# Kernel optimization log

Measured on AMD Instinct MI355X. Metric: run time of the kernel, lower is better.

Reference implementation:

```python
import jax, jax.numpy as jnp
import numpy as np

B, S, D, H, DFF, NL, VOCAB, SRC = 16, 128, 768, 12, 3072, 6, 32000, 256


def _pe_table():
    pos = np.arange(S)[:, None].astype(np.float32)
    div = np.exp(np.arange(0, D, 2).astype(np.float32) * (-np.log(10000.0) / D))
    pe = np.zeros((S, D), np.float32)
    pe[:, 0::2] = np.sin(pos * div)
    pe[:, 1::2] = np.cos(pos * div)
    return jnp.asarray(pe)


def _ln(x, a, b, eps=1e-6):
    m = jnp.mean(x, axis=-1, keepdims=True)
    v = jnp.mean((x - m) ** 2, axis=-1, keepdims=True)
    return a * (x - m) / jnp.sqrt(v + eps) + b


def _mha(q_in, k_in, v_in, mask, Wq, bq, Wk, bk, Wv, bv, Wo, bo):
    Bq, Sq, Dm = q_in.shape
    Sk = k_in.shape[1]
    dk = Dm // H
    q = (q_in @ Wq + bq).reshape(Bq, Sq, H, dk).transpose(0, 2, 1, 3)
    k = (k_in @ Wk + bk).reshape(Bq, Sk, H, dk).transpose(0, 2, 1, 3)
    v = (v_in @ Wv + bv).reshape(Bq, Sk, H, dk).transpose(0, 2, 1, 3)
    s = jnp.einsum('bhqd,bhkd->bhqk', q, k) / jnp.sqrt(jnp.float32(dk))
    if mask is not None:
        s = jnp.where(mask == 0, jnp.float32(-1e9), s)
    a = jax.nn.softmax(s, axis=-1)
    o = jnp.einsum('bhqk,bhkd->bhqd', a, v).transpose(0, 2, 1, 3).reshape(Bq, Sq, Dm)
    return o @ Wo + bo


def _combined_mask(trg):
    # Vectorized, faithful replica of create_combined_mask (incl. its cumulative
    # cross-batch zeroing: for j in 0..B-2, if padding_start[j]!=0 zero rows
    # >= padding_start[j] of ALL batches b >= j).
    b, s = trg.shape
    is_pad = (trg == 0)
    haspad = jnp.any(is_pad, axis=1)
    start = jnp.where(haspad, jnp.argmax(is_pad, axis=1), 0)  # first pad idx, 0 if none
    c = jnp.where(start == 0, s + 1, start)                   # sentinel = never cut
    cmin = jax.lax.cummin(c)
    r = cmin[jnp.minimum(jnp.arange(b), b - 2)]               # effective cutoff per batch
    look = jnp.tril(jnp.ones((s, s), jnp.float32))
    keep = (jnp.arange(s)[None, :] < r[:, None]).astype(jnp.float32)  # (B,S) rows kept
    return (look[None] * keep[:, :, None])[:, None]           # (B,1,S,S)


def setup_inputs():
    key = jax.random.key(0)
    ks = jax.random.split(key, 16)
    tok = jax.random.randint(ks[0], (B, S), 1, VOCAB)
    lens = jax.random.randint(ks[1], (B,), S // 2, S + 1)
    trg = jnp.where(jnp.arange(S)[None, :] < lens[:, None], tok, 0).astype(jnp.int32)
    e_outputs = jax.random.normal(ks[2], (B, SRC, D), dtype=jnp.float32)
    src_mask = jax.random.randint(ks[3], (B, 1, 1, SRC), 0, 2).at[..., 0].set(1).astype(jnp.int32)
    w = lambda k, shape: (jax.random.normal(k, shape) * 0.02).astype(jnp.float32)
    emb = (jax.random.normal(ks[4], (VOCAB, D)) * 0.1).astype(jnp.float32).at[0].set(0.0)
    return {
        'trg': trg, 'e_outputs': e_outputs, 'src_mask': src_mask,
        'emb': emb,
        'y_param': jax.random.normal(ks[5], (S, D), dtype=jnp.float32),
        'pe_alpha': jnp.float32(1.0),
        'Wq': w(ks[6], (NL, 3, D, D)), 'Wk': w(ks[7], (NL, 3, D, D)),
        'Wv': w(ks[8], (NL, 3, D, D)), 'Wo': w(ks[9], (NL, 3, D, D)),
        'bq': jnp.zeros((NL, 3, D)), 'bk': jnp.zeros((NL, 3, D)),
        'bv': jnp.zeros((NL, 3, D)), 'bo': jnp.zeros((NL, 3, D)),
        'W1': w(ks[10], (NL, D, DFF)), 'b1': jnp.zeros((NL, DFF)),
        'W2': w(ks[11], (NL, DFF, D)), 'b2': jnp.zeros((NL, D)),
        'ln_a': jnp.ones((NL, 5, D)), 'ln_b': jnp.zeros((NL, 5, D)),
        'final_a': jnp.ones((D,)), 'final_b': jnp.zeros((D,)),
    }


def reference(trg, e_outputs, src_mask, emb, y_param, pe_alpha, Wq, Wk, Wv, Wo,
              bq, bk, bv, bo, W1, b1, W2, b2, ln_a, ln_b, final_a, final_b):
    x = emb[trg] + pe_alpha * _pe_table()            # embedding + scaled PE
    y = jnp.broadcast_to(y_param, (trg.shape[0],) + y_param.shape)
    trg_mask = _combined_mask(trg)
    for i in range(Wq.shape[0]):
        x2 = _ln(x, ln_a[i, 0], ln_b[i, 0])
        x = x + _mha(x2, x2, x2, trg_mask, Wq[i, 0], bq[i, 0], Wk[i, 0], bk[i, 0], Wv[i, 0], bv[i, 0], Wo[i, 0], bo[i, 0])
        y2 = _ln(y, ln_a[i, 1], ln_b[i, 1])
        y = y + _mha(y2, e_outputs, e_outputs, src_mask, Wq[i, 1], bq[i, 1], Wk[i, 1], bk[i, 1], Wv[i, 1], bv[i, 1], Wo[i, 1], bo[i, 1])
        x2 = _ln(x, ln_a[i, 2], ln_b[i, 2])
        y3 = _ln(y, ln_a[i, 3], ln_b[i, 3])
        x = x + _mha(x2, y3, y3, None, Wq[i, 2], bq[i, 2], Wk[i, 2], bk[i, 2], Wv[i, 2], bv[i, 2], Wo[i, 2], bo[i, 2])
        x2 = _ln(x, ln_a[i, 4], ln_b[i, 4])
        x = x + jnp.maximum(x2 @ W1[i] + b1[i], 0.0) @ W2[i] + b2[i]
    return _ln(x, final_a, final_b)
```

## Files before the change

### kernel.cpp

```cpp
#include <hip/hip_runtime.h>

#define BB 16
#define SS 128
#define DD 768
#define HH 12
#define DKK 64
#define DFFF 3072
#define NLL 6
#define SRCC 256

typedef short bf16x8 __attribute__((ext_vector_type(8)));
typedef float f32x4 __attribute__((ext_vector_type(4)));
typedef unsigned short us8 __attribute__((ext_vector_type(8)));
typedef unsigned short us4 __attribute__((ext_vector_type(4)));

__device__ __forceinline__ unsigned short f2bf(float f) {
  unsigned int u = __builtin_bit_cast(unsigned int, f);
  u = (u + 0x7fff + ((u >> 16) & 1)) >> 16;
  return (unsigned short)u;
}

#define GLOADLDS16(gp, lp)                                              \
  __builtin_amdgcn_global_load_lds(                                     \
      (const __attribute__((address_space(1))) void*)(gp),              \
      (__attribute__((address_space(3))) void*)(lp), 16, 0, 0)

__global__ void pe_build_k(float* __restrict__ pe) {
  int idx = blockIdx.x * blockDim.x + threadIdx.x;
  if (idx >= SS * (DD / 2)) return;
  int s = idx / (DD / 2);
  int i = idx - s * (DD / 2);
  float div = expf((float)(2 * i) * (-logf(10000.0f) / (float)DD));
  float ang = (float)s * div;
  pe[s * DD + 2 * i]     = sinf(ang);
  pe[s * DD + 2 * i + 1] = cosf(ang);
}

__global__ void embjoint_k(const int* __restrict__ trg, const float* __restrict__ emb,
                           const float* __restrict__ pe, const float* __restrict__ alpha,
                           const float* __restrict__ yp,
                           float* __restrict__ x, float* __restrict__ y) {
  int idx = blockIdx.x * blockDim.x + threadIdx.x;
  int c = idx % (DD / 4);
  int r = idx / (DD / 4);
  if (r >= BB * SS) return;
  int s = r % SS;
  if (blockIdx.y == 0) {
    float al = alpha[0];
    float4 e = *(const float4*)(emb + (size_t)trg[r] * DD + c * 4);
    float4 p = *(const float4*)(pe + (size_t)s * DD + c * 4);
    float4 o;
    o.x = e.x + al * p.x; o.y = e.y + al * p.y;
    o.z = e.z + al * p.z; o.w = e.w + al * p.w;
    *(float4*)(x + (size_t)r * DD + c * 4) = o;
  } else {
    *(float4*)(y + (size_t)r * DD + c * 4) = *(const float4*)(yp + (size_t)s * DD + c * 4);
  }
}

__global__ void mb_k(const int* __restrict__ trg, int* __restrict__ rbuf,
                     const float* __restrict__ bq, const float* __restrict__ bk,
                     const float* __restrict__ bv, float* __restrict__ bqkv1,
                     float* __restrict__ bkv2, float* __restrict__ bqkv3) {
  int t = threadIdx.x;
  if (blockIdx.x == 0) {
    __shared__ int first[BB];
    if (t < BB) first[t] = 0x7fffffff;
    __syncthreads();
    int b = t >> 4, p0 = (t & 15) * 8;
    int loc = 0x7fffffff;
#pragma unroll
    for (int i = 0; i < 8; i++) {
      if (trg[b * SS + p0 + i] == 0) { loc = p0 + i; break; }
    }
    atomicMin(&first[b], loc);
    __syncthreads();
    if (t == 0) {
      int cmin = 0x7fffffff;
      int cm[BB];
      for (int bb = 0; bb < BB; bb++) {
        int start = (first[bb] == 0x7fffffff) ? 0 : first[bb];
        int c = (start == 0) ? (SS + 1) : start;
        cmin = min(cmin, c);
        cm[bb] = cmin;
      }
      for (int bb = 0; bb < BB; bb++) rbuf[bb] = cm[min(bb, BB - 2)];
    }
    return;
  }
  int i = (blockIdx.x - 1) * 256 + t;
  if (i >= NLL * 6144) return;
  int l = i / 6144, j = i - l * 6144;
  if (j < 2304) {
    int s = j / 768, c = j - s * 768;
    const float* src = (s == 0) ? bq : (s == 1 ? bk : bv);
    bqkv1[l * 2304 + j] = src[(l * 3 + 0) * 768 + c];
  } else if (j < 3840) {
    int jj = j - 2304;
    int s = jj / 768, c = jj - s * 768;
    bkv2[l * 1536 + jj] = ((s == 0) ? bk : bv)[(l * 3 + 1) * 768 + c];
  } else {
    int jj = j - 3840;
    int s = jj / 768, c = jj - s * 768;
    const float* src = (s == 0) ? bq : (s == 1 ? bk : bv);
    bqkv3[l * 2304 + jj] = src[(l * 3 + 2) * 768 + c];
  }
}

__global__ __launch_bounds__(256) void ln_k(const float* __restrict__ x,
                                            const float* __restrict__ ga,
                                            const float* __restrict__ gb,
                                            float* __restrict__ out) {
  __shared__ float sm[8];
  int row = blockIdx.x;
  int t = threadIdx.x;
  const float* xr = x + (size_t)row * DD;
  float v0 = xr[t], v1 = xr[t + 256], v2 = xr[t + 512];
  float s = v0 + v1 + v2;
#pragma unroll
  for (int o = 32; o > 0; o >>= 1) s += __shfl_down(s, o);
  if ((t & 63) == 0) sm[t >> 6] = s;
  __syncthreads();
  float mean = (sm[0] + sm[1] + sm[2] + sm[3]) * (1.0f / (float)DD);
  float d0 = v0 - mean, d1 = v1 - mean, d2 = v2 - mean;
  float q = d0 * d0 + d1 * d1 + d2 * d2;
#pragma unroll
  for (int o = 32; o > 0; o >>= 1) q += __shfl_down(q, o);
  if ((t & 63) == 0) sm[4 + (t >> 6)] = q;
  __syncthreads();
  float var = (sm[4] + sm[5] + sm[6] + sm[7]) * (1.0f / (float)DD);
  float inv = 1.0f / sqrtf(var + 1e-6f);
  float* orow = out + (size_t)row * DD;
  orow[t]       = ga[t] * d0 * inv + gb[t];
  orow[t + 256] = ga[t + 256] * d1 * inv + gb[t + 256];
  orow[t + 512] = ga[t + 512] * d2 * inv + gb[t + 512];
}

__device__ __forceinline__ void lnb_body(const float* __restrict__ xr,
                                         const float* __restrict__ ga,
                                         const float* __restrict__ gb,
                                         unsigned short* __restrict__ orow,
                                         float* sm, int t) {
  float v0 = xr[t], v1 = xr[t + 256], v2 = xr[t + 512];
  float s = v0 + v1 + v2;
#pragma unroll
  for (int o = 32; o > 0; o >>= 1) s += __shfl_down(s, o);
  if ((t & 63) == 0) sm[t >> 6] = s;
  __syncthreads();
  float mean = (sm[0] + sm[1] + sm[2] + sm[3]) * (1.0f / (float)DD);
  float d0 = v0 - mean, d1 = v1 - mean, d2 = v2 - mean;
  float q = d0 * d0 + d1 * d1 + d2 * d2;
#pragma unroll
  for (int o = 32; o > 0; o >>= 1) q += __shfl_down(q, o);
  if ((t & 63) == 0) sm[4 + (t >> 6)] = q;
  __syncthreads();
  float var = (sm[4] + sm[5] + sm[6] + sm[7]) * (1.0f / (float)DD);
  float inv = 1.0f / sqrtf(var + 1e-6f);
  orow[t]       = f2bf(ga[t] * d0 * inv + gb[t]);
  orow[t + 256] = f2bf(ga[t + 256] * d1 * inv + gb[t + 256]);
  orow[t + 512] = f2bf(ga[t + 512] * d2 * inv + gb[t + 512]);
}

__global__ __launch_bounds__(256) void lnb_k(const float* __restrict__ x,
                                             const float* __restrict__ ga,
                                             const float* __restrict__ gb,
                                             unsigned short* __restrict__ out) {
  __shared__ float sm[8];
  int row = blockIdx.x;
  lnb_body(x + (size_t)row * DD, ga, gb, out + (size_t)row * DD, sm, threadIdx.x);
}

__global__ __launch_bounds__(256) void lnb2_k(const float* __restrict__ x,
                                              const float* __restrict__ y,
                                              const float* __restrict__ ga2,
                                              const float* __restrict__ gb2,
                                              const float* __restrict__ ga3,
                                              const float* __restrict__ gb3,
                                              unsigned short* __restrict__ ox,
                                              unsigned short* __restrict__ oy) {
  __shared__ float sm[8];
  int row = blockIdx.x;
  if (row < BB * SS)
    lnb_body(x + (size_t)row * DD, ga2, gb2, ox + (size_t)row * DD, sm, threadIdx.x);
  else {
    row -= BB * SS;
    lnb_body(y + (size_t)row * DD, ga3, gb3, oy + (size_t)row * DD, sm, threadIdx.x);
  }
}

__device__ __forceinline__ void wt_tile(const float* __restrict__ s,
                                        unsigned short* __restrict__ d,
                                        int K, int N, int k0, int n0,
                                        float (*tl)[65], int t) {
  int rr = t >> 4, cc = (t & 15) * 4;
#pragma unroll
  for (int i = 0; i < 4; i++) {
    int row = rr + i * 16;
    float4 v = *(const float4*)(s + (size_t)(k0 + row) * N + n0 + cc);
    tl[row][cc + 0] = v.x; tl[row][cc + 1] = v.y;
    tl[row][cc + 2] = v.z; tl[row][cc + 3] = v.w;
  }
  __syncthreads();
  int kchunk = t & 7, nrow = t >> 3;
#pragma unroll
  for (int p = 0; p < 2; p++) {
    int n = p * 32 + nrow;
    us8 o;
#pragma unroll
    for (int j = 0; j < 8; j++) o[j] = f2bf(tl[kchunk * 8 + j][n]);
    *(us8*)(d + (size_t)(n0 + n) * K + k0 + kchunk * 8) = o;
  }
}

__global__ __launch_bounds__(256) void wt_k(const float* __restrict__ src,
                                            unsigned short* __restrict__ dst,
                                            int K, int N) {
  __shared__ float tl[64][65];
  wt_tile(src + (size_t)blockIdx.z * K * N, dst + (size_t)blockIdx.z * K * N,
          K, N, blockIdx.y * 64, blockIdx.x * 64, tl, threadIdx.x);
}

__global__ __launch_bounds__(256) void wtall_k(
    const float* __restrict__ Wq, const float* __restrict__ Wk,
    const float* __restrict__ Wv, const float* __restrict__ Wo,
    unsigned short* __restrict__ wqkv1A, unsigned short* __restrict__ wq2A,
    unsigned short* __restrict__ wkv2A, unsigned short* __restrict__ wqkv3A,
    unsigned short* __restrict__ wotA) {
  __shared__ float tl[64][65];
  const size_t M1 = (size_t)DD * DD;
  int z = blockIdx.z;
  int l = z / 12, m = z - l * 12;
  size_t s3 = (size_t)l * 3 * M1;
  const float* s;
  unsigned short* d;
  switch (m) {
    case 0:  s = Wq + s3;          d = wqkv1A + l * 3 * M1;          break;
    case 1:  s = Wk + s3;          d = wqkv1A + l * 3 * M1 + M1;     break;
    case 2:  s = Wv + s3;          d = wqkv1A + l * 3 * M1 + 2 * M1; break;
    case 3:  s = Wq + s3 + M1;     d = wq2A + l * M1;                break;
    case 4:  s = Wk + s3 + M1;     d = wkv2A + l * 2 * M1;           break;
    case 5:  s = Wv + s3 + M1;     d = wkv2A + l * 2 * M1 + M1;      break;
    case 6:  s = Wq + s3 + 2 * M1; d = wqkv3A + l * 3 * M1;          break;
    case 7:  s = Wk + s3 + 2 * M1; d = wqkv3A + l * 3 * M1 + M1;     break;
    case 8:  s = Wv + s3 + 2 * M1; d = wqkv3A + l * 3 * M1 + 2 * M1; break;
    case 9:  s = Wo + s3;          d = wotA + l * 3 * M1;            break;
    case 10: s = Wo + s3 + M1;     d = wotA + l * 3 * M1 + M1;       break;
    default: s = Wo + s3 + 2 * M1; d = wotA + l * 3 * M1 + 2 * M1;   break;
  }
  wt_tile(s, d, DD, DD, blockIdx.y * 64, blockIdx.x * 64, tl, threadIdx.x);
}

__global__ void cvt_k(const float* __restrict__ s, unsigned short* __restrict__ d, int n8) {
  int i = blockIdx.x * blockDim.x + threadIdx.x;
  if (i >= n8) return;
  float4 a = *(const float4*)(s + (size_t)i * 8);
  float4 b = *(const float4*)(s + (size_t)i * 8 + 4);
  us8 o;
  o[0] = f2bf(a.x); o[1] = f2bf(a.y); o[2] = f2bf(a.z); o[3] = f2bf(a.w);
  o[4] = f2bf(b.x); o[5] = f2bf(b.y); o[6] = f2bf(b.z); o[7] = f2bf(b.w);
  *(us8*)(d + (size_t)i * 8) = o;
}

template <int BM>
__global__ __launch_bounds__(256) void mgemm_k(
    const unsigned short* __restrict__ A0, const unsigned short* __restrict__ A1,
    const unsigned short* __restrict__ Bt, const float* __restrict__ bias,
    const float* __restrict__ res, void* __restrict__ C,
    unsigned short* __restrict__ hd0, unsigned short* __restrict__ hd1,
    unsigned short* __restrict__ hd2,
    int sh0, int sh1, int sh2, int M, int N, int K, int flags, int vtbits) {
  constexpr int FM = BM / 32;
  constexpr int HB = BM / 2;
  __shared__ unsigned short As[BM * 32];
  __shared__ unsigned short Bs[64 * 32];
  int t = threadIdx.x;
  int wave = t >> 6, lane = t & 63;
  int m0 = blockIdx.y * BM, n0 = blockIdx.x * 64;
  int seg = n0 / 768;
  const unsigned short* A = (seg == 0) ? A0 : A1;
  int wm = wave >> 1, wn = wave & 1;
  f32x4 acc[FM][2] = {};
  int aRow = t >> 2, aC8 = (t & 3) * 8;
  const unsigned short* Ab = A + (size_t)m0 * K + aC8;
  const unsigned short* Bb = Bt + (size_t)n0 * K + aC8;
  int aOff0 = (wm * HB + (lane & 15)) * 32 + (lane >> 4) * 8;
  int bOff0 = (wn * 32 + (lane & 15)) * 32 + (lane >> 4) * 8;
  for (int k0 = 0; k0 < K; k0 += 32) {
#pragma unroll
    for (int h = 0; h < BM / 64; h++)
      GLOADLDS16(Ab + (size_t)(h * 64 + aRow) * K + k0, As + h * 2048 + wave * 512);
    GLOADLDS16(Bb + (size_t)aRow * K + k0, Bs + wave * 512);
    __syncthreads();
    bf16x8 aF[FM], bF[2];
#pragma unroll
    for (int fm = 0; fm < FM; fm++)
      aF[fm] = *(const bf16x8*)(As + aOff0 + fm * 16 * 32);
#pragma unroll
    for (int fn = 0; fn < 2; fn++)
      bF[fn] = *(const bf16x8*)(Bs + bOff0 + fn * 16 * 32);
#pragma unroll
    for (int fm = 0; fm < FM; fm++)
#pragma unroll
      for (int fn = 0; fn < 2; fn++)
        acc[fm][fn] = __builtin_amdgcn_mfma_f32_16x16x32_bf16(aF[fm], bF[fn], acc[fm][fn], 0, 0, 0);
    __syncthreads();
  }
  int lcol = lane & 15, lrow4 = (lane >> 4) * 4;
  bool hm = (flags & 4) != 0;
  unsigned short* hd = nullptr;
  int sh = 0, segBase = seg * 768, vtseg = 0;
  if (hm) {
    hd = (seg == 0) ? hd0 : (seg == 1 ? hd1 : hd2);
    sh = (seg == 0) ? sh0 : (seg == 1 ? sh1 : sh2);
    vtseg = (vtbits >> seg) & 1;
  }
#pragma unroll
  for (int fm = 0; fm < FM; fm++) {
#pragma unroll
    for (int fn = 0; fn < 2; fn++) {
      int col = n0 + wn * 32 + fn * 16 + lcol;
      float bv = bias[col];
      int rowb = m0 + wm * HB + fm * 16 + lrow4;
      if (hm) {
        int colr = col - segBase;
        int hh = colr >> 6, dd = colr & 63;
        int bb = rowb >> sh, ssb = rowb & ((1 << sh) - 1);
        if (vtseg) {
          size_t idx = (((size_t)bb * HH + hh) * 64 + dd) * (size_t)(1 << sh) + ssb;
          us4 pk;
#pragma unroll
          for (int r = 0; r < 4; r++) pk[r] = f2bf(acc[fm][fn][r] + bv);
          *(us4*)(hd + idx) = pk;
        } else {
          size_t base = ((((size_t)bb * HH + hh) << sh) + ssb) * 64 + dd;
#pragma unroll
          for (int r = 0; r < 4; r++) hd[base + (size_t)r * 64] = f2bf(acc[fm][fn][r] + bv);
        }
      } else {
#pragma unroll
        for (int r = 0; r < 4; r++) {
          int row = rowb + r;
          float v = acc[fm][fn][r] + bv;
          size_t idx = (size_t)row * N + col;
          if (res) v += res[idx];
          if (flags & 1) v = fmaxf(v, 0.f);
          if (flags & 2) ((unsigned short*)C)[idx] = f2bf(v);
          else ((float*)C)[idx] = v;
        }
      }
    }
  }
}

template <int SK>
__global__ __launch_bounds__(256) void attn3_k(const unsigned short* __restrict__ qh,
                                               const unsigned short* __restrict__ kh,
                                               const unsigned short* __restrict__ vth,
                                               unsigned short* __restrict__ ctxb, int mode,
                                               const int* __restrict__ rbuf,
                                               const int* __restrict__ smask) {
  constexpr int NPH = SK / 128;
  constexpr int NF = SK / 16;
  __shared__ unsigned short kvb[128 * 72];
  __shared__ unsigned short pbuf[64 * (SK + 8)];
  int qhalf = blockIdx.x, h = blockIdx.y, b = blockIdx.z;
  int t = threadIdx.x;
  int wave = t >> 6, lane = t & 63;
  int l15 = lane & 15, lhi = lane >> 4;
  int qrow0 = qhalf * 64 + wave * 16;
  size_t bh = (size_t)b * HH + h;
  bf16x8 aQ[2];
#pragma unroll
  for (int ks = 0; ks < 2; ks++)
    aQ[ks] = *(const bf16x8*)(qh + (bh * SS + qrow0 + l15) * 64 + ks * 32 + lhi * 8);
  f32x4 accS[NF] = {};
  const unsigned short* kbase = kh + bh * SK * 64;
  for (int ph = 0; ph < NPH; ph++) {
    if (ph) __syncthreads();
    {
      int c0 = t * 4;
#pragma unroll
      for (int i = 0; i < 4; i++) {
        int c = c0 + i, row = c >> 3, co = (c & 7) * 8;
        *(us8*)&kvb[row * 72 + co] = *(const us8*)(kbase + (size_t)(ph * 128 + row) * 64 + co);
      }
    }
    __syncthreads();
#pragma unroll
    for (int kf = 0; kf < 8; kf++) {
      int gf = ph * 8 + kf;
#pragma unroll
      for (int ks = 0; ks < 2; ks++) {
        bf16x8 bK = *(const bf16x8*)(&kvb[(kf * 16 + l15) * 72 + ks * 32 + lhi * 8]);
        accS[gf] = __builtin_amdgcn_mfma_f32_16x16x32_bf16(aQ[ks], bK, accS[gf], 0, 0, 0);
      }
    }
  }
  int rcut = (mode == 0) ? rbuf[b] : 0;
#pragma unroll
  for (int r = 0; r < 4; r++) {
    int qg = qrow0 + lhi * 4 + r;
    float mx = -3.4e38f;
#pragma unroll
    for (int gf = 0; gf < NF; gf++) {
      int k = gf * 16 + l15;
      float s = accS[gf][r] * 0.125f;
      bool keep = true;
      if (mode == 0) keep = (k <= qg) && (qg < rcut);
      else if (mode == 1) keep = (smask[b * SRCC + k] != 0);
      s = keep ? s : -1e9f;
      accS[gf][r] = s;
      mx = fmaxf(mx, s);
    }
#pragma unroll
    for (int o = 1; o < 16; o <<= 1) mx = fmaxf(mx, __shfl_xor(mx, o));
    float sum = 0.f;
#pragma unroll
    for (int gf = 0; gf < NF; gf++) {
      float e = expf(accS[gf][r] - mx);
      accS[gf][r] = e;
      sum += e;
    }
#pragma unroll
    for (int o = 1; o < 16; o <<= 1) sum += __shfl_xor(sum, o);
    float rinv = 1.0f / sum;
#pragma unroll
    for (int gf = 0; gf < NF; gf++) accS[gf][r] *= rinv;
  }
#pragma unroll
  for (int gf = 0; gf < NF; gf++) {
#pragma unroll
    for (int r = 0; r < 4; r++) {
      int ql = wave * 16 + lhi * 4 + r;
      pbuf[ql * (SK + 8) + gf * 16 + l15] = f2bf(accS[gf][r]);
    }
  }
  __syncthreads();
  f32x4 accO[4] = {};
  const unsigned short* vbase = vth + bh * 64 * SK;
  for (int ph = 0; ph < NPH; ph++) {
    if (ph) __syncthreads();
    {
      int c0 = t * 4;
#pragma unroll
      for (int i = 0; i < 4; i++) {
        int c = c0 + i, row = c >> 4, co = (c & 15) * 8;
        *(us8*)&kvb[row * 136 + co] = *(const us8*)(vbase + (size_t)row * SK + ph * 128 + co);
      }
    }
    __syncthreads();
#pragma unroll
    for (int ks = 0; ks < 4; ks++) {
      bf16x8 aP = *(const bf16x8*)(&pbuf[(wave * 16 + l15) * (SK + 8) + ph * 128 + ks * 32 + lhi * 8]);
#pragma unroll
      for (int nf = 0; nf < 4; nf++) {
        bf16x8 bV = *(const bf16x8*)(&kvb[(nf * 16 + l15) * 136 + ks * 32 + lhi * 8]);
        accO[nf] = __builtin_amdgcn_mfma_f32_16x16x32_bf16(aP, bV, accO[nf], 0, 0, 0);
      }
    }
  }
#pragma unroll
  for (int nf = 0; nf < 4; nf++) {
#pragma unroll
    for (int r = 0; r < 4; r++) {
      int qg = qrow0 + lhi * 4 + r;
      ctxb[((size_t)b * SS + qg) * DD + h * 64 + nf * 16 + l15] = f2bf(accO[nf][r]);
    }
  }
}

extern "C" void kernel_launch(void* const* d_in, const int* in_sizes, int n_in,
                              void* d_out, int out_size, void* d_ws, size_t ws_size,
                              hipStream_t stream) {
  const int*   trg   = (const int*)d_in[0];
  const float* e_out = (const float*)d_in[1];
  const int*   smask = (const int*)d_in[2];
  const float* emb   = (const float*)d_in[3];
  const float* ypar  = (const float*)d_in[4];
  const float* alpha = (const float*)d_in[5];
  const float* Wq = (const float*)d_in[6];
  const float* Wk = (const float*)d_in[7];
  const float* Wv = (const float*)d_in[8];
  const float* Wo = (const float*)d_in[9];
  const float* bq = (const float*)d_in[10];
  const float* bk = (const float*)d_in[11];
  const float* bv = (const float*)d_in[12];
  const float* bo = (const float*)d_in[13];
  const float* W1 = (const float*)d_in[14];
  const float* b1 = (const float*)d_in[15];
  const float* W2 = (const float*)d_in[16];
  const float* b2 = (const float*)d_in[17];
  const float* lna = (const float*)d_in[18];
  const float* lnbp = (const float*)d_in[19];
  const float* fa = (const float*)d_in[20];
  const float* fb = (const float*)d_in[21];
  float* out = (float*)d_out;

  float* ws = (float*)d_ws;
  size_t off = 0;
  auto alloc = [&](size_t n) { float* p = ws + off; off += n; return p; };
  const size_t M1 = (size_t)DD * DD;
  float* pe  = alloc((size_t)SS * DD);
  int* rbuf  = (int*)alloc(64);
  float* x   = alloc((size_t)BB * SS * DD);
  float* y   = alloc((size_t)BB * SS * DD);
  float* bqkv1 = alloc((size_t)NLL * 2304);
  float* bkv2  = alloc((size_t)NLL * 1536);
  float* bqkv3 = alloc((size_t)NLL * 2304);
  unsigned short* qhb  = (unsigned short*)alloc((size_t)BB * HH * SS * DKK / 2);
  unsigned short* khb  = (unsigned short*)alloc((size_t)BB * HH * SRCC * DKK / 2);
  unsigned short* vthb = (unsigned short*)alloc((size_t)BB * HH * SRCC * DKK / 2);
  unsigned short* x2b   = (unsigned short*)alloc((size_t)BB * SS * DD / 2);
  unsigned short* y3b   = (unsigned short*)alloc((size_t)BB * SS * DD / 2);
  unsigned short* ctxb  = (unsigned short*)alloc((size_t)BB * SS * DD / 2);
  unsigned short* midb  = (unsigned short*)alloc((size_t)BB * SS * DFFF / 2);
  unsigned short* eob   = (unsigned short*)alloc((size_t)BB * SRCC * DD / 2);
  unsigned short* wqkv1A = (unsigned short*)alloc((size_t)NLL * 3 * M1 / 2);
  unsigned short* wq2A   = (unsigned short*)alloc((size_t)NLL * M1 / 2);
  unsigned short* wkv2A  = (unsigned short*)alloc((size_t)NLL * 2 * M1 / 2);
  unsigned short* wqkv3A = (unsigned short*)alloc((size_t)NLL * 3 * M1 / 2);
  unsigned short* wotA   = (unsigned short*)alloc((size_t)NLL * 3 * M1 / 2);
  unsigned short* w1tA   = (unsigned short*)alloc((size_t)NLL * DD * DFFF / 2);
  unsigned short* w2tA   = (unsigned short*)alloc((size_t)NLL * DFFF * DD / 2);
  if (ws_size < off * sizeof(float)) return;

  pe_build_k<<<(SS * (DD / 2) + 255) / 256, 256, 0, stream>>>(pe);
  embjoint_k<<<dim3((BB * SS * (DD / 4) + 255) / 256, 2), 256, 0, stream>>>(
      trg, emb, pe, alpha, ypar, x, y);
  mb_k<<<1 + (NLL * 6144 + 255) / 256, 256, 0, stream>>>(trg, rbuf, bq, bk, bv,
                                                         bqkv1, bkv2, bqkv3);
  cvt_k<<<(BB * SRCC * DD / 8 + 255) / 256, 256, 0, stream>>>(e_out, eob, BB * SRCC * DD / 8);
  wtall_k<<<dim3(12, 12, NLL * 12), 256, 0, stream>>>(Wq, Wk, Wv, Wo,
                                                      wqkv1A, wq2A, wkv2A, wqkv3A, wotA);
  wt_k<<<dim3(48, 12, NLL), 256, 0, stream>>>(W1, w1tA, DD, DFFF);
  wt_k<<<dim3(12, 48, NLL), 256, 0, stream>>>(W2, w2tA, DFFF, DD);

  auto MG128 = [&](const unsigned short* A0, const unsigned short* A1, int M, int K,
                   const unsigned short* Bt, int N, const float* bias, const float* res,
                   void* C, unsigned short* h0, unsigned short* h1, unsigned short* h2,
                   int s0, int s1, int s2, int flags, int vtb) {
    mgemm_k<128><<<dim3(N / 64, M / 128), 256, 0, stream>>>(A0, A1, Bt, bias, res, C,
                                                            h0, h1, h2, s0, s1, s2, M, N, K, flags, vtb);
  };
  auto MG64 = [&](const unsigned short* A0, int M, int K,
                  const unsigned short* Bt, int N, const float* bias, const float* res,
                  void* C, unsigned short* h0, int s0, int flags, int vtb) {
    mgemm_k<64><<<dim3(N / 64, M / 64), 256, 0, stream>>>(A0, A0, Bt, bias, res, C,
                                                          h0, nullptr, nullptr, s0, 0, 0, M, N, K, flags, vtb);
  };
  const dim3 agrid(SS / 64, HH, BB);

  for (int l = 0; l < NLL; l++) {
    auto LNB = [&](const float* in, int slot, unsigned short* o) {
      lnb_k<<<BB * SS, 256, 0, stream>>>(in, lna + ((size_t)l * 5 + slot) * DD,
                                         lnbp + ((size_t)l * 5 + slot) * DD, o);
    };
    LNB(x, 0, x2b);
    MG128(x2b, x2b, BB * SS, DD, wqkv1A + l * 3 * M1, 2304, bqkv1 + l * 2304, nullptr,
          nullptr, qhb, khb, vthb, 7, 7, 7, 4, 0b100);
    attn3_k<SS><<<agrid, 256, 0, stream>>>(qhb, khb, vthb, ctxb, 0, rbuf, nullptr);
    MG64(ctxb, BB * SS, DD, wotA + l * 3 * M1, DD, bo + ((size_t)l * 3 + 0) * DD, x, x,
         nullptr, 0, 0, 0);
    LNB(y, 1, x2b);
    MG64(x2b, BB * SS, DD, wq2A + l * M1, DD, bq + ((size_t)l * 3 + 1) * DD, nullptr,
         nullptr, qhb, 7, 4, 1 * 0);
    MG128(eob, eob, BB * SRCC, DD, wkv2A + l * 2 * M1, 1536, bkv2 + l * 1536, nullptr,
          nullptr, khb, vthb, nullptr, 8, 8, 0, 4, 0b10);
    attn3_k<SRCC><<<agrid, 256, 0, stream>>>(qhb, khb, vthb, ctxb, 1, nullptr, smask);
    MG64(ctxb, BB * SS, DD, wotA + l * 3 * M1 + M1, DD, bo + ((size_t)l * 3 + 1) * DD, y, y,
         nullptr, 0, 0, 0);
    lnb2_k<<<2 * BB * SS, 256, 0, stream>>>(x, y,
        lna + ((size_t)l * 5 + 2) * DD, lnbp + ((size_t)l * 5 + 2) * DD,
        lna + ((size_t)l * 5 + 3) * DD, lnbp + ((size_t)l * 5 + 3) * DD, x2b, y3b);
    MG128(x2b, y3b, BB * SS, DD, wqkv3A + l * 3 * M1, 2304, bqkv3 + l * 2304, nullptr,
          nullptr, qhb, khb, vthb, 7, 7, 7, 4, 0b100);
    attn3_k<SS><<<agrid, 256, 0, stream>>>(qhb, khb, vthb, ctxb, 2, nullptr, nullptr);
    MG64(ctxb, BB * SS, DD, wotA + l * 3 * M1 + 2 * M1, DD, bo + ((size_t)l * 3 + 2) * DD, x, x,
         nullptr, 0, 0, 0);
    LNB(x, 4, x2b);
    MG128(x2b, x2b, BB * SS, DD, w1tA + (size_t)l * DD * DFFF, DFFF, b1 + (size_t)l * DFFF,
          nullptr, midb, nullptr, nullptr, nullptr, 0, 0, 0, 3, 0);
    MG64(midb, BB * SS, DFFF, w2tA + (size_t)l * DFFF * DD, DD, b2 + (size_t)l * DD, x, x,
         nullptr, 0, 0, 0);
  }
  ln_k<<<BB * SS, 256, 0, stream>>>(x, fa, fb, out);
}
```

Measured before the change: 1.653 ms.

## Batch independent self/cross attention branches and precompute cross-attention K/V for all layers

The self-attention and cross-attention branches in each layer are independent, so their LayerNorms, Q/QKV projections and output projections are now fused into shared launches (lnb2_k, qkvq_k, wob_k). The encoder K/V projections for all six layers are computed up front in one large GEMM launch instead of once per layer. All weight transposes and the e_out conversion are merged into a single kernel with larger tiles, and the PE table is computed inline during embedding. This cuts launch count and gives small GEMMs more blocks for occupancy, at the cost of extra workspace for per-layer K/V buffers.

```diff
diff --git a/kernel.cpp b/kernel.cpp
--- a/kernel.cpp
+++ b/kernel.cpp
@@ -1,4 +1,5 @@
 #include <hip/hip_runtime.h>
+#include <math.h>
 
 #define BB 16
 #define SS 128
@@ -25,19 +26,8 @@
       (const __attribute__((address_space(1))) void*)(gp),              \
       (__attribute__((address_space(3))) void*)(lp), 16, 0, 0)
 
-__global__ void pe_build_k(float* __restrict__ pe) {
-  int idx = blockIdx.x * blockDim.x + threadIdx.x;
-  if (idx >= SS * (DD / 2)) return;
-  int s = idx / (DD / 2);
-  int i = idx - s * (DD / 2);
-  float div = expf((float)(2 * i) * (-logf(10000.0f) / (float)DD));
-  float ang = (float)s * div;
-  pe[s * DD + 2 * i]     = sinf(ang);
-  pe[s * DD + 2 * i + 1] = cosf(ang);
-}
-
 __global__ void embjoint_k(const int* __restrict__ trg, const float* __restrict__ emb,
-                           const float* __restrict__ pe, const float* __restrict__ alpha,
+                           const float* __restrict__ alpha,
                            const float* __restrict__ yp,
                            float* __restrict__ x, float* __restrict__ y) {
   int idx = blockIdx.x * blockDim.x + threadIdx.x;
@@ -48,10 +38,15 @@
   if (blockIdx.y == 0) {
     float al = alpha[0];
     float4 e = *(const float4*)(emb + (size_t)trg[r] * DD + c * 4);
-    float4 p = *(const float4*)(pe + (size_t)s * DD + c * 4);
+    float coef = -logf(10000.0f) / (float)DD;
+    float div0 = expf((float)(4 * c) * coef);
+    float div1 = expf((float)(4 * c + 2) * coef);
+    float s0, c0, s1, c1;
+    sincosf((float)s * div0, &s0, &c0);
+    sincosf((float)s * div1, &s1, &c1);
     float4 o;
-    o.x = e.x + al * p.x; o.y = e.y + al * p.y;
-    o.z = e.z + al * p.z; o.w = e.w + al * p.w;
+    o.x = e.x + al * s0; o.y = e.y + al * c0;
+    o.z = e.z + al * s1; o.w = e.w + al * c1;
     *(float4*)(x + (size_t)r * DD + c * 4) = o;
   } else {
     *(float4*)(y + (size_t)r * DD + c * 4) = *(const float4*)(yp + (size_t)s * DD + c * 4);
@@ -172,93 +167,156 @@
 
 __global__ __launch_bounds__(256) void lnb2_k(const float* __restrict__ x,
                                               const float* __restrict__ y,
-                                              const float* __restrict__ ga2,
-                                              const float* __restrict__ gb2,
-                                              const float* __restrict__ ga3,
-                                              const float* __restrict__ gb3,
+                                              const float* __restrict__ gax,
+                                              const float* __restrict__ gbx,
+                                              const float* __restrict__ gay,
+                                              const float* __restrict__ gby,
                                               unsigned short* __restrict__ ox,
                                               unsigned short* __restrict__ oy) {
   __shared__ float sm[8];
   int row = blockIdx.x;
   if (row < BB * SS)
-    lnb_body(x + (size_t)row * DD, ga2, gb2, ox + (size_t)row * DD, sm, threadIdx.x);
+    lnb_body(x + (size_t)row * DD, gax, gbx, ox + (size_t)row * DD, sm, threadIdx.x);
   else {
     row -= BB * SS;
-    lnb_body(y + (size_t)row * DD, ga3, gb3, oy + (size_t)row * DD, sm, threadIdx.x);
-  }
-}
-
-__device__ __forceinline__ void wt_tile(const float* __restrict__ s,
+    lnb_body(y + (size_t)row * DD, gay, gby, oy + (size_t)row * DD, sm, threadIdx.x);
+  }
+}
+
+__device__ __forceinline__ void tr_tile(const float* __restrict__ s,
                                         unsigned short* __restrict__ d,
                                         int K, int N, int k0, int n0,
-                                        float (*tl)[65], int t) {
-  int rr = t >> 4, cc = (t & 15) * 4;
+                                        float (*tl)[69], int t) {
+#pragma unroll
+  for (int i = 0; i < 8; i++) {
+    int c = t + i * 256;
+    int row = c >> 4, c4 = (c & 15) * 4;
+    float4 v = *(const float4*)(s + (size_t)(k0 + row) * N + n0 + c4);
+    tl[row][c4 + 0] = v.x; tl[row][c4 + 1] = v.y;
+    tl[row][c4 + 2] = v.z; tl[row][c4 + 3] = v.w;
+  }
+  __syncthreads();
 #pragma unroll
   for (int i = 0; i < 4; i++) {
-    int row = rr + i * 16;
-    float4 v = *(const float4*)(s + (size_t)(k0 + row) * N + n0 + cc);
-    tl[row][cc + 0] = v.x; tl[row][cc + 1] = v.y;
-    tl[row][cc + 2] = v.z; tl[row][cc + 3] = v.w;
-  }
-  __syncthreads();
-  int kchunk = t & 7, nrow = t >> 3;
-#pragma unroll
-  for (int p = 0; p < 2; p++) {
-    int n = p * 32 + nrow;
+    int c = t + i * 256;
+    int n = c >> 4, kc = c & 15;
     us8 o;
 #pragma unroll
-    for (int j = 0; j < 8; j++) o[j] = f2bf(tl[kchunk * 8 + j][n]);
-    *(us8*)(d + (size_t)(n0 + n) * K + k0 + kchunk * 8) = o;
-  }
-}
-
-__global__ __launch_bounds__(256) void wt_k(const float* __restrict__ src,
-                                            unsigned short* __restrict__ dst,
-                                            int K, int N) {
-  __shared__ float tl[64][65];
-  wt_tile(src + (size_t)blockIdx.z * K * N, dst + (size_t)blockIdx.z * K * N,
-          K, N, blockIdx.y * 64, blockIdx.x * 64, tl, threadIdx.x);
-}
-
-__global__ __launch_bounds__(256) void wtall_k(
+    for (int j = 0; j < 8; j++) o[j] = f2bf(tl[kc * 8 + j][n]);
+    *(us8*)(d + (size_t)(n0 + n) * K + k0 + kc * 8) = o;
+  }
+}
+
+__global__ __launch_bounds__(256) void wtx_k(
     const float* __restrict__ Wq, const float* __restrict__ Wk,
     const float* __restrict__ Wv, const float* __restrict__ Wo,
+    const float* __restrict__ W1, const float* __restrict__ W2,
+    const float* __restrict__ e_out,
     unsigned short* __restrict__ wqkv1A, unsigned short* __restrict__ wq2A,
     unsigned short* __restrict__ wkv2A, unsigned short* __restrict__ wqkv3A,
-    unsigned short* __restrict__ wotA) {
-  __shared__ float tl[64][65];
+    unsigned short* __restrict__ wotA,
+    unsigned short* __restrict__ w1tA, unsigned short* __restrict__ w2tA,
+    unsigned short* __restrict__ eob) {
+  __shared__ float tl[128][69];
   const size_t M1 = (size_t)DD * DD;
-  int z = blockIdx.z;
-  int l = z / 12, m = z - l * 12;
-  size_t s3 = (size_t)l * 3 * M1;
-  const float* s;
-  unsigned short* d;
-  switch (m) {
-    case 0:  s = Wq + s3;          d = wqkv1A + l * 3 * M1;          break;
-    case 1:  s = Wk + s3;          d = wqkv1A + l * 3 * M1 + M1;     break;
-    case 2:  s = Wv + s3;          d = wqkv1A + l * 3 * M1 + 2 * M1; break;
-    case 3:  s = Wq + s3 + M1;     d = wq2A + l * M1;                break;
-    case 4:  s = Wk + s3 + M1;     d = wkv2A + l * 2 * M1;           break;
-    case 5:  s = Wv + s3 + M1;     d = wkv2A + l * 2 * M1 + M1;      break;
-    case 6:  s = Wq + s3 + 2 * M1; d = wqkv3A + l * 3 * M1;          break;
-    case 7:  s = Wk + s3 + 2 * M1; d = wqkv3A + l * 3 * M1 + M1;     break;
-    case 8:  s = Wv + s3 + 2 * M1; d = wqkv3A + l * 3 * M1 + 2 * M1; break;
-    case 9:  s = Wo + s3;          d = wotA + l * 3 * M1;            break;
-    case 10: s = Wo + s3 + M1;     d = wotA + l * 3 * M1 + M1;       break;
-    default: s = Wo + s3 + 2 * M1; d = wotA + l * 3 * M1 + 2 * M1;   break;
-  }
-  wt_tile(s, d, DD, DD, blockIdx.y * 64, blockIdx.x * 64, tl, threadIdx.x);
-}
-
-__global__ void cvt_k(const float* __restrict__ s, unsigned short* __restrict__ d, int n8) {
-  int i = blockIdx.x * blockDim.x + threadIdx.x;
-  if (i >= n8) return;
-  float4 a = *(const float4*)(s + (size_t)i * 8);
-  float4 b = *(const float4*)(s + (size_t)i * 8 + 4);
-  us8 o;
-  o[0] = f2bf(a.x); o[1] = f2bf(a.y); o[2] = f2bf(a.z); o[3] = f2bf(a.w);
-  o[4] = f2bf(b.x); o[5] = f2bf(b.y); o[6] = f2bf(b.z); o[7] = f2bf(b.w);
-  *(us8*)(d + (size_t)i * 8) = o;
+  int bid = blockIdx.x;
+  int t = threadIdx.x;
+  if (bid < 5184) {
+    int mat = bid / 72, rem = bid % 72;
+    int kt = rem / 12, nt = rem % 12;
+    int l = mat / 12, m = mat % 12;
+    size_t s3 = (size_t)l * 3 * M1;
+    const float* s;
+    unsigned short* d;
+    switch (m) {
+      case 0:  s = Wq + s3;          d = wqkv1A + l * 3 * M1;          break;
+      case 1:  s = Wk + s3;          d = wqkv1A + l * 3 * M1 + M1;     break;
+      case 2:  s = Wv + s3;          d = wqkv1A + l * 3 * M1 + 2 * M1; break;
+      case 3:  s = Wq + s3 + M1;     d = wq2A + l * M1;                break;
+      case 4:  s = Wk + s3 + M1;     d = wkv2A + l * 2 * M1;           break;
+      case 5:  s = Wv + s3 + M1;     d = wkv2A + l * 2 * M1 + M1;      break;
+      case 6:  s = Wq + s3 + 2 * M1; d = wqkv3A + l * 3 * M1;          break;
+      case 7:  s = Wk + s3 + 2 * M1; d = wqkv3A + l * 3 * M1 + M1;     break;
+      case 8:  s = Wv + s3 + 2 * M1; d = wqkv3A + l * 3 * M1 + 2 * M1; break;
+      case 9:  s = Wo + s3;          d = wotA + l * 3 * M1;            break;
+      case 10: s = Wo + s3 + M1;     d = wotA + l * 3 * M1 + M1;       break;
+      default: s = Wo + s3 + 2 * M1; d = wotA + l * 3 * M1 + 2 * M1;   break;
+    }
+    tr_tile(s, d, DD, DD, kt * 128, nt * 64, tl, t);
+  } else if (bid < 6912) {
+    int idx = bid - 5184;
+    int l = idx / 288, rem = idx % 288;
+    int kt = rem / 48, nt = rem % 48;
+    tr_tile(W1 + (size_t)l * DD * DFFF, w1tA + (size_t)l * DD * DFFF,
+            DD, DFFF, kt * 128, nt * 64, tl, t);
+  } else if (bid < 8640) {
+    int idx = bid - 6912;
+    int l = idx / 288, rem = idx % 288;
+    int kt = rem / 12, nt = rem % 12;
+    tr_tile(W2 + (size_t)l * DFFF * DD, w2tA + (size_t)l * DFFF * DD,
+            DFFF, DD, kt * 128, nt * 64, tl, t);
+  } else {
+    size_t base = (size_t)(bid - 8640) * 2048 + (size_t)t * 8;
+    float4 a = *(const float4*)(e_out + base);
+    float4 b = *(const float4*)(e_out + base + 4);
+    us8 o;
+    o[0] = f2bf(a.x); o[1] = f2bf(a.y); o[2] = f2bf(a.z); o[3] = f2bf(a.w);
+    o[4] = f2bf(b.x); o[5] = f2bf(b.y); o[6] = f2bf(b.z); o[7] = f2bf(b.w);
+    *(us8*)(eob + base) = o;
+  }
+}
+
+#define GEMM_BODY(BM, A, Bt, m0, n0)                                          \
+  constexpr int FM = (BM) / 32;                                               \
+  constexpr int HB = (BM) / 2;                                                \
+  int wave = t >> 6, lane = t & 63;                                           \
+  int wm = wave >> 1, wn = wave & 1;                                          \
+  f32x4 acc[FM][2] = {};                                                      \
+  int aRow = t >> 2, aC8 = (t & 3) * 8;                                       \
+  const unsigned short* Ab = (A) + (size_t)(m0)*768 + aC8;                    \
+  const unsigned short* Bb = (Bt) + (size_t)(n0)*768 + aC8;                   \
+  int aOff0 = (wm * HB + (lane & 15)) * 32 + (lane >> 4) * 8;                 \
+  int bOff0 = (wn * 32 + (lane & 15)) * 32 + (lane >> 4) * 8;                 \
+  for (int k0 = 0; k0 < 768; k0 += 32) {                                      \
+    _Pragma("unroll")                                                         \
+    for (int h = 0; h < (BM) / 64; h++)                                       \
+      GLOADLDS16(Ab + (size_t)(h * 64 + aRow) * 768 + k0,                     \
+                 As + h * 2048 + wave * 512);                                 \
+    GLOADLDS16(Bb + (size_t)aRow * 768 + k0, Bs + wave * 512);                \
+    __syncthreads();                                                          \
+    bf16x8 aF[FM], bF[2];                                                     \
+    _Pragma("unroll")                                                         \
+    for (int fm = 0; fm < FM; fm++)                                           \
+      aF[fm] = *(const bf16x8*)(As + aOff0 + fm * 16 * 32);                   \
+    _Pragma("unroll")                                                         \
+    for (int fn = 0; fn < 2; fn++)                                            \
+      bF[fn] = *(const bf16x8*)(Bs + bOff0 + fn * 16 * 32);                   \
+    _Pragma("unroll")                                                         \
+    for (int fm = 0; fm < FM; fm++)                                           \
+      _Pragma("unroll")                                                       \
+      for (int fn = 0; fn < 2; fn++)                                          \
+        acc[fm][fn] = __builtin_amdgcn_mfma_f32_16x16x32_bf16(                \
+            aF[fm], bF[fn], acc[fm][fn], 0, 0, 0);                            \
+    __syncthreads();                                                          \
+  }                                                                           \
+  int lcol = lane & 15, lrow4 = (lane >> 4) * 4;
+
+__device__ __forceinline__ void hm_store(unsigned short* hd, int sh, int vt,
+                                         int rowb, int colr, const f32x4& a,
+                                         float bv) {
+  int hh = colr >> 6, dd = colr & 63;
+  int bb = rowb >> sh, ssb = rowb & ((1 << sh) - 1);
+  if (vt) {
+    size_t idx = (((size_t)bb * HH + hh) * 64 + dd) * (size_t)(1 << sh) + ssb;
+    us4 pk;
+#pragma unroll
+    for (int r = 0; r < 4; r++) pk[r] = f2bf(a[r] + bv);
+    *(us4*)(hd + idx) = pk;
+  } else {
+    size_t base = ((((size_t)bb * HH + hh) << sh) + ssb) * 64 + dd;
+#pragma unroll
+    for (int r = 0; r < 4; r++) hd[base + (size_t)r * 64] = f2bf(a[r] + bv);
+  }
 }
 
 template <int BM>
@@ -322,20 +380,7 @@
       float bv = bias[col];
       int rowb = m0 + wm * HB + fm * 16 + lrow4;
       if (hm) {
-        int colr = col - segBase;
-        int hh = colr >> 6, dd = colr & 63;
-        int bb = rowb >> sh, ssb = rowb & ((1 << sh) - 1);
-        if (vtseg) {
-          size_t idx = (((size_t)bb * HH + hh) * 64 + dd) * (size_t)(1 << sh) + ssb;
-          us4 pk;
-#pragma unroll
-          for (int r = 0; r < 4; r++) pk[r] = f2bf(acc[fm][fn][r] + bv);
-          *(us4*)(hd + idx) = pk;
-        } else {
-          size_t base = ((((size_t)bb * HH + hh) << sh) + ssb) * 64 + dd;
-#pragma unroll
-          for (int r = 0; r < 4; r++) hd[base + (size_t)r * 64] = f2bf(acc[fm][fn][r] + bv);
-        }
+        hm_store(hd, sh, vtseg, rowb, col - segBase, acc[fm][fn], bv);
       } else {
 #pragma unroll
         for (int r = 0; r < 4; r++) {
@@ -347,6 +392,102 @@
           if (flags & 2) ((unsigned short*)C)[idx] = f2bf(v);
           else ((float*)C)[idx] = v;
         }
+      }
+    }
+  }
+}
+
+__global__ __launch_bounds__(256) void kv2all_k(
+    const unsigned short* __restrict__ eob, const unsigned short* __restrict__ wkv2A,
+    const float* __restrict__ bkv2,
+    unsigned short* __restrict__ khb2A, unsigned short* __restrict__ vthb2A) {
+  __shared__ unsigned short As[128 * 32];
+  __shared__ unsigned short Bs[64 * 32];
+  const size_t M1 = (size_t)DD * DD;
+  const size_t KVS = (size_t)BB * HH * SRCC * DKK;
+  int t = threadIdx.x;
+  int l = blockIdx.z;
+  int m0 = blockIdx.y * 128, n0 = blockIdx.x * 64;
+  const unsigned short* Bt = wkv2A + (size_t)l * 2 * M1;
+  const float* bias = bkv2 + l * 1536;
+  GEMM_BODY(128, eob, Bt, m0, n0)
+  int seg = n0 / 768;
+  unsigned short* hd = (seg == 0) ? khb2A + (size_t)l * KVS : vthb2A + (size_t)l * KVS;
+  int vt = seg;
+  int segBase = seg * 768;
+#pragma unroll
+  for (int fm = 0; fm < FM; fm++) {
+#pragma unroll
+    for (int fn = 0; fn < 2; fn++) {
+      int col = n0 + wn * 32 + fn * 16 + lcol;
+      int rowb = m0 + wm * HB + fm * 16 + lrow4;
+      hm_store(hd, 8, vt, rowb, col - segBase, acc[fm][fn], bias[col]);
+    }
+  }
+}
+
+__global__ __launch_bounds__(256) void qkvq_k(
+    const unsigned short* __restrict__ x2b, const unsigned short* __restrict__ y1b,
+    const unsigned short* __restrict__ Bqkv, const unsigned short* __restrict__ Bq2,
+    const float* __restrict__ bias1, const float* __restrict__ bias2,
+    unsigned short* __restrict__ qhb, unsigned short* __restrict__ khb,
+    unsigned short* __restrict__ vthb, unsigned short* __restrict__ qhb2) {
+  __shared__ unsigned short As[128 * 32];
+  __shared__ unsigned short Bs[64 * 32];
+  int t = threadIdx.x;
+  int bid = blockIdx.x;
+  bool j1 = bid >= 576;
+  int bx, by;
+  const unsigned short *A, *Bt;
+  const float* bias;
+  if (!j1) { bx = bid % 36; by = bid / 36; A = x2b; Bt = Bqkv; bias = bias1; }
+  else { int b2 = bid - 576; bx = b2 % 12; by = b2 / 12; A = y1b; Bt = Bq2; bias = bias2; }
+  int m0 = by * 128, n0 = bx * 64;
+  GEMM_BODY(128, A, Bt, m0, n0)
+  int seg = j1 ? 0 : (n0 / 768);
+  unsigned short* hd = j1 ? qhb2 : (seg == 0 ? qhb : (seg == 1 ? khb : vthb));
+  int vt = (!j1 && seg == 2) ? 1 : 0;
+  int segBase = seg * 768;
+#pragma unroll
+  for (int fm = 0; fm < FM; fm++) {
+#pragma unroll
+    for (int fn = 0; fn < 2; fn++) {
+      int col = n0 + wn * 32 + fn * 16 + lcol;
+      int rowb = m0 + wm * HB + fm * 16 + lrow4;
+      hm_store(hd, 7, vt, rowb, col - segBase, acc[fm][fn], bias[col]);
+    }
+  }
+}
+
+__global__ __launch_bounds__(256) void wob_k(
+    const unsigned short* __restrict__ ctx1b, const unsigned short* __restrict__ ctx2b,
+    const unsigned short* __restrict__ Bt0, const unsigned short* __restrict__ Bt1,
+    const float* __restrict__ bo0, const float* __restrict__ bo1,
+    float* __restrict__ x, float* __restrict__ y) {
+  __shared__ unsigned short As[64 * 32];
+  __shared__ unsigned short Bs[64 * 32];
+  int t = threadIdx.x;
+  int bid = blockIdx.x;
+  bool j1 = bid >= 384;
+  int b2 = j1 ? bid - 384 : bid;
+  int bx = b2 % 12, by = b2 / 12;
+  const unsigned short* A = j1 ? ctx2b : ctx1b;
+  const unsigned short* Bt = j1 ? Bt1 : Bt0;
+  const float* bias = j1 ? bo1 : bo0;
+  float* C = j1 ? y : x;
+  int m0 = by * 64, n0 = bx * 64;
+  GEMM_BODY(64, A, Bt, m0, n0)
+#pragma unroll
+  for (int fm = 0; fm < FM; fm++) {
+#pragma unroll
+    for (int fn = 0; fn < 2; fn++) {
+      int col = n0 + wn * 32 + fn * 16 + lcol;
+      float bv = bias[col];
+      int rowb = m0 + wm * HB + fm * 16 + lrow4;
+#pragma unroll
+      for (int r = 0; r < 4; r++) {
+        size_t idx = (size_t)(rowb + r) * DD + col;
+        C[idx] += acc[fm][fn][r] + bv;
       }
     }
   }
@@ -500,19 +641,23 @@
   size_t off = 0;
   auto alloc = [&](size_t n) { float* p = ws + off; off += n; return p; };
   const size_t M1 = (size_t)DD * DD;
-  float* pe  = alloc((size_t)SS * DD);
+  const size_t KVS = (size_t)BB * HH * SRCC * DKK;
   int* rbuf  = (int*)alloc(64);
   float* x   = alloc((size_t)BB * SS * DD);
   float* y   = alloc((size_t)BB * SS * DD);
   float* bqkv1 = alloc((size_t)NLL * 2304);
   float* bkv2  = alloc((size_t)NLL * 1536);
   float* bqkv3 = alloc((size_t)NLL * 2304);
-  unsigned short* qhb  = (unsigned short*)alloc((size_t)BB * HH * SS * DKK / 2);
-  unsigned short* khb  = (unsigned short*)alloc((size_t)BB * HH * SRCC * DKK / 2);
-  unsigned short* vthb = (unsigned short*)alloc((size_t)BB * HH * SRCC * DKK / 2);
+  unsigned short* qhb   = (unsigned short*)alloc((size_t)BB * HH * SS * DKK / 2);
+  unsigned short* qhb2  = (unsigned short*)alloc((size_t)BB * HH * SS * DKK / 2);
+  unsigned short* khb   = (unsigned short*)alloc((size_t)BB * HH * SS * DKK / 2);
+  unsigned short* vthb  = (unsigned short*)alloc((size_t)BB * HH * SS * DKK / 2);
+  unsigned short* khb2A  = (unsigned short*)alloc((size_t)NLL * KVS / 2);
+  unsigned short* vthb2A = (unsigned short*)alloc((size_t)NLL * KVS / 2);
   unsigned short* x2b   = (unsigned short*)alloc((size_t)BB * SS * DD / 2);
   unsigned short* y3b   = (unsigned short*)alloc((size_t)BB * SS * DD / 2);
-  unsigned short* ctxb  = (unsigned short*)alloc((size_t)BB * SS * DD / 2);
+  unsigned short* ctx1b = (unsigned short*)alloc((size_t)BB * SS * DD / 2);
+  unsigned short* ctx2b = (unsigned short*)alloc((size_t)BB * SS * DD / 2);
   unsigned short* midb  = (unsigned short*)alloc((size_t)BB * SS * DFFF / 2);
   unsigned short* eob   = (unsigned short*)alloc((size_t)BB * SRCC * DD / 2);
   unsigned short* wqkv1A = (unsigned short*)alloc((size_t)NLL * 3 * M1 / 2);
@@ -524,16 +669,13 @@
   unsigned short* w2tA   = (unsigned short*)alloc((size_t)NLL * DFFF * DD / 2);
   if (ws_size < off * sizeof(float)) return;
 
-  pe_build_k<<<(SS * (DD / 2) + 255) / 256, 256, 0, stream>>>(pe);
   embjoint_k<<<dim3((BB * SS * (DD / 4) + 255) / 256, 2), 256, 0, stream>>>(
-      trg, emb, pe, alpha, ypar, x, y);
+      trg, emb, alpha, ypar, x, y);
   mb_k<<<1 + (NLL * 6144 + 255) / 256, 256, 0, stream>>>(trg, rbuf, bq, bk, bv,
                                                          bqkv1, bkv2, bqkv3);
-  cvt_k<<<(BB * SRCC * DD / 8 + 255) / 256, 256, 0, stream>>>(e_out, eob, BB * SRCC * DD / 8);
-  wtall_k<<<dim3(12, 12, NLL * 12), 256, 0, stream>>>(Wq, Wk, Wv, Wo,
-                                                      wqkv1A, wq2A, wkv2A, wqkv3A, wotA);
-  wt_k<<<dim3(48, 12, NLL), 256, 0, stream>>>(W1, w1tA, DD, DFFF);
-  wt_k<<<dim3(12, 48, NLL), 256, 0, stream>>>(W2, w2tA, DFFF, DD);
+  wtx_k<<<10176, 256, 0, stream>>>(Wq, Wk, Wv, Wo, W1, W2, e_out,
+                                   wqkv1A, wq2A, wkv2A, wqkv3A, wotA, w1tA, w2tA, eob);
+  kv2all_k<<<dim3(24, 32, NLL), 256, 0, stream>>>(eob, wkv2A, bkv2, khb2A, vthb2A);
 
   auto MG128 = [&](const unsigned short* A0, const unsigned short* A1, int M, int K,
                    const unsigned short* Bt, int N, const float* bias, const float* res,
@@ -551,33 +693,25 @@
   const dim3 agrid(SS / 64, HH, BB);
 
   for (int l = 0; l < NLL; l++) {
-    auto LNB = [&](const float* in, int slot, unsigned short* o) {
-      lnb_k<<<BB * SS, 256, 0, stream>>>(in, lna + ((size_t)l * 5 + slot) * DD,
-                                         lnbp + ((size_t)l * 5 + slot) * DD, o);
-    };
-    LNB(x, 0, x2b);
-    MG128(x2b, x2b, BB * SS, DD, wqkv1A + l * 3 * M1, 2304, bqkv1 + l * 2304, nullptr,
-          nullptr, qhb, khb, vthb, 7, 7, 7, 4, 0b100);
-    attn3_k<SS><<<agrid, 256, 0, stream>>>(qhb, khb, vthb, ctxb, 0, rbuf, nullptr);
-    MG64(ctxb, BB * SS, DD, wotA + l * 3 * M1, DD, bo + ((size_t)l * 3 + 0) * DD, x, x,
-         nullptr, 0, 0, 0);
-    LNB(y, 1, x2b);
-    MG64(x2b, BB * SS, DD, wq2A + l * M1, DD, bq + ((size_t)l * 3 + 1) * DD, nullptr,
-         nullptr, qhb, 7, 4, 1 * 0);
-    MG128(eob, eob, BB * SRCC, DD, wkv2A + l * 2 * M1, 1536, bkv2 + l * 1536, nullptr,
-          nullptr, khb, vthb, nullptr, 8, 8, 0, 4, 0b10);
-    attn3_k<SRCC><<<agrid, 256, 0, stream>>>(qhb, khb, vthb, ctxb, 1, nullptr, smask);
-    MG64(ctxb, BB * SS, DD, wotA + l * 3 * M1 + M1, DD, bo + ((size_t)l * 3 + 1) * DD, y, y,
-         nullptr, 0, 0, 0);
-    lnb2_k<<<2 * BB * SS, 256, 0, stream>>>(x, y,
-        lna + ((size_t)l * 5 + 2) * DD, lnbp + ((size_t)l * 5 + 2) * DD,
-        lna + ((size_t)l * 5 + 3) * DD, lnbp + ((size_t)l * 5 + 3) * DD, x2b, y3b);
+    const float* lA = lna + (size_t)l * 5 * DD;
+    const float* lB = lnbp + (size_t)l * 5 * DD;
+    lnb2_k<<<2 * BB * SS, 256, 0, stream>>>(x, y, lA, lB, lA + DD, lB + DD, x2b, y3b);
+    qkvq_k<<<768, 256, 0, stream>>>(x2b, y3b, wqkv1A + l * 3 * M1, wq2A + l * M1,
+                                    bqkv1 + l * 2304, bq + ((size_t)l * 3 + 1) * DD,
+                                    qhb, khb, vthb, qhb2);
+    attn3_k<SS><<<agrid, 256, 0, stream>>>(qhb, khb, vthb, ctx1b, 0, rbuf, nullptr);
+    attn3_k<SRCC><<<agrid, 256, 0, stream>>>(qhb2, khb2A + l * KVS, vthb2A + l * KVS,
+                                             ctx2b, 1, nullptr, smask);
+    wob_k<<<768, 256, 0, stream>>>(ctx1b, ctx2b, wotA + l * 3 * M1, wotA + l * 3 * M1 + M1,
+                                   bo + (size_t)l * 3 * DD, bo + ((size_t)l * 3 + 1) * DD, x, y);
+    lnb2_k<<<2 * BB * SS, 256, 0, stream>>>(x, y, lA + 2 * DD, lB + 2 * DD,
+                                            lA + 3 * DD, lB + 3 * DD, x2b, y3b);
     MG128(x2b, y3b, BB * SS, DD, wqkv3A + l * 3 * M1, 2304, bqkv3 + l * 2304, nullptr,
           nullptr, qhb, khb, vthb, 7, 7, 7, 4, 0b100);
-    attn3_k<SS><<<agrid, 256, 0, stream>>>(qhb, khb, vthb, ctxb, 2, nullptr, nullptr);
-    MG64(ctxb, BB * SS, DD, wotA + l * 3 * M1 + 2 * M1, DD, bo + ((size_t)l * 3 + 2) * DD, x, x,
-         nullptr, 0, 0, 0);
-    LNB(x, 4, x2b);
+    attn3_k<SS><<<agrid, 256, 0, stream>>>(qhb, khb, vthb, ctx1b, 2, nullptr, nullptr);
+    MG64(ctx1b, BB * SS, DD, wotA + l * 3 * M1 + 2 * M1, DD, bo + ((size_t)l * 3 + 2) * DD,
+         x, x, nullptr, 0, 0, 0);
+    lnb_k<<<BB * SS, 256, 0, stream>>>(x, lA + 4 * DD, lB + 4 * DD, x2b);
     MG128(x2b, x2b, BB * SS, DD, w1tA + (size_t)l * DD * DFFF, DFFF, b1 + (size_t)l * DFFF,
           nullptr, midb, nullptr, nullptr, nullptr, 0, 0, 0, 3, 0);
     MG64(midb, BB * SS, DFFF, w2tA + (size_t)l * DFFF * DD, DD, b2 + (size_t)l * DD, x, x,
```

Result: faster. 1.529 ms (-7.5%).
